# Performance work log

Hardware: AMD Instinct MI355X
Metric: run time of the kernel (lower is better)

Reference implementation:

```python
import jax, jax.numpy as jnp
import numpy as np

ODE_UNFOLDS = 6
EPS = 1e-8


def setup_inputs() -> dict:
    key = jax.random.key(0)
    ks = jax.random.split(key, 16)
    B, T, IN, U = 256, 128, 64, 256

    def unif(k, shape, lo, hi):
        return jax.random.uniform(k, shape, jnp.float32, lo, hi)

    def pm1(k, shape):  # random +/-1 reversal potentials (as in ncps erev init)
        return (2.0 * jax.random.bernoulli(k, 0.5, shape) - 1.0).astype(jnp.float32)

    return {
        "x_ltc": jax.random.normal(ks[0], (B, T, IN), jnp.float32),
        "timespans": jnp.ones((B, T, 1), jnp.float32),
        # sensory synapses (input -> units)
        "sensory_mu": unif(ks[1], (IN, U), 0.3, 0.8),
        "sensory_sigma": unif(ks[2], (IN, U), 3.0, 8.0),
        "sensory_w": unif(ks[3], (IN, U), 0.001, 1.0),
        "sensory_erev": pm1(ks[4], (IN, U)),
        # recurrent synapses (units -> units)
        "mu": unif(ks[5], (U, U), 0.3, 0.8),
        "sigma": unif(ks[6], (U, U), 3.0, 8.0),
        "w": unif(ks[7], (U, U), 0.001, 1.0),
        "erev": pm1(ks[8], (U, U)),
        # per-neuron leak / capacitance
        "gleak": unif(ks[9], (U,), 0.001, 1.0),
        "vleak": unif(ks[10], (U,), -0.2, 0.2),
        "cm": unif(ks[11], (U,), 0.4, 0.6),
        # affine input / output mappings
        "input_w": jnp.ones((IN,), jnp.float32),
        "input_b": jnp.zeros((IN,), jnp.float32),
        "output_w": jnp.ones((U,), jnp.float32),
        "output_b": jnp.zeros((U,), jnp.float32),
        # head: Linear(hidden, 1)
        "head_w": jax.random.normal(ks[12], (1, U), jnp.float32) * 0.05,
        "head_b": jnp.zeros((1,), jnp.float32),
    }


def reference(x_ltc, timespans, sensory_mu, sensory_sigma, sensory_w, sensory_erev,
              mu, sigma, w, erev, gleak, vleak, cm,
              input_w, input_b, output_w, output_b, head_w, head_b):
    B = x_ltc.shape[0]
    U = gleak.shape[0]

    def gate(v, mu_, sigma_):
        # v: (B, pre) -> (B, pre, post) sigmoid activation
        return jax.nn.sigmoid(sigma_ * (v[:, :, None] - mu_))

    def cell(v, xt, elapsed):
        x = xt * input_w + input_b                              # (B, IN)
        s_act = sensory_w * gate(x, sensory_mu, sensory_sigma)  # (B, IN, U)
        w_num_s = jnp.sum(s_act * sensory_erev, axis=1)          # (B, U)
        w_den_s = jnp.sum(s_act, axis=1)                         # (B, U)
        cm_t = cm / (elapsed / ODE_UNFOLDS)                      # (B, U) via (B,1) bcast
        for _ in range(ODE_UNFOLDS):                             # semi-implicit Euler unfolds
            w_act = w * gate(v, mu, sigma)                       # (B, U, U)
            w_num = jnp.sum(w_act * erev, axis=1) + w_num_s
            w_den = jnp.sum(w_act, axis=1) + w_den_s
            num = cm_t * v + gleak * vleak + w_num
            den = cm_t + gleak + w_den
            v = num / (den + EPS)
        return v

    def step(v, inp):
        xt, el = inp
        return cell(v, xt, el), None

    v0 = jnp.zeros((B, U), x_ltc.dtype)
    xs = (jnp.swapaxes(x_ltc, 0, 1), jnp.swapaxes(timespans, 0, 1))  # (T,B,IN), (T,B,1)
    vT, _ = jax.lax.scan(step, v0, xs)
    h_out = vT * output_w + output_b                             # output mapping of last step
    return h_out @ head_w.T + head_b                             # (B, 1)
```

## Files before the change

kernel.cpp:

```cpp
#include <hip/hip_runtime.h>
#include <hip/hip_bf16.h>
#include <hip/hip_fp16.h>

#define LOG2E 1.4426950408889634f

constexpr int B_ = 256, T_ = 128, IN_ = 64, U_ = 256;
constexpr int UNFOLDS = 6;

constexpr size_t OFF_RCD = 0;
constexpr size_t OFF_RWS = 262144;
constexpr size_t OFF_SCD = 393216;
constexpr size_t OFF_SWS = 458752;
constexpr size_t OFF_ELF = 491520;
constexpr size_t OFF_VEC = 622592;

typedef _Float16 hv2 __attribute__((ext_vector_type(2)));

__device__ __forceinline__ float ldf(const void* p, int idx, bool isbf) {
  return isbf ? __bfloat162float(((const __hip_bfloat16*)p)[idx])
              : ((const float*)p)[idx];
}

__device__ __forceinline__ float fdot2f(__half2 a, __half2 b, float c) {
#if __has_builtin(__builtin_amdgcn_fdot2)
  return __builtin_amdgcn_fdot2(__builtin_bit_cast(hv2, a),
                                __builtin_bit_cast(hv2, b), c, false);
#else
  return c + __low2float(a) * __low2float(b) +
         __high2float(a) * __high2float(b);
#endif
}

__device__ __forceinline__ unsigned packpair(float lo, float hi) {
  return __builtin_bit_cast(unsigned, __builtin_amdgcn_cvt_pkrtz(lo, hi));
}

__global__ __launch_bounds__(256) void ltc_prep(
    const void* tspan, const void* smu, const void* ssigma, const void* sw,
    const void* serev, const void* mu, const void* sigma, const void* w,
    const void* erev, const void* gleak, const void* vleak, const void* cm,
    const void* inw, const void* inb, const void* outw, const void* outb,
    const void* headw, const void* headb, char* __restrict__ ws) {
  const bool isbf = (((const unsigned*)tspan)[0] == 0x3F803F80u);
  const int idx = blockIdx.x * blockDim.x + threadIdx.x;

  uint2*    rcd = (uint2*)(ws + OFF_RCD);
  unsigned* rws = (unsigned*)(ws + OFF_RWS);
  uint2*    scd = (uint2*)(ws + OFF_SCD);
  unsigned* sws = (unsigned*)(ws + OFF_SWS);
  float*    elf = (float*)(ws + OFF_ELF);
  float*    vec = (float*)(ws + OFF_VEC);

  if (idx < (U_ * U_) / 2) {
    const int j = idx & 255, P = idx >> 8;
    const int e0 = (2 * P) * U_ + j, e1 = (2 * P + 1) * U_ + j;
    float sg0 = ldf(sigma, e0, isbf), m0 = ldf(mu, e0, isbf);
    float w0  = ldf(w, e0, isbf),     er0 = ldf(erev, e0, isbf);
    float sg1 = ldf(sigma, e1, isbf), m1 = ldf(mu, e1, isbf);
    float w1  = ldf(w, e1, isbf),     er1 = ldf(erev, e1, isbf);
    __half2 C, D, W;
    C.x = __float2half_rn(sg0 * m0 * LOG2E);  C.y = __float2half_rn(sg1 * m1 * LOG2E);
    D.x = __float2half_rn(-sg0 * LOG2E);      D.y = __float2half_rn(-sg1 * LOG2E);
    W.x = __float2half_rn(w0 * er0);          W.y = __float2half_rn(w1 * er1);
    rcd[P * 256 + j] = make_uint2(__builtin_bit_cast(unsigned, C),
                                  __builtin_bit_cast(unsigned, D));
    rws[P * 256 + j] = __builtin_bit_cast(unsigned, W);
  }
  if (idx < (IN_ * U_) / 2) {
    const int j = idx & 255, P = idx >> 8;
    const int e0 = (2 * P) * U_ + j, e1 = (2 * P + 1) * U_ + j;
    float sg0 = ldf(ssigma, e0, isbf), m0 = ldf(smu, e0, isbf);
    float w0  = ldf(sw, e0, isbf),     er0 = ldf(serev, e0, isbf);
    float sg1 = ldf(ssigma, e1, isbf), m1 = ldf(smu, e1, isbf);
    float w1  = ldf(sw, e1, isbf),     er1 = ldf(serev, e1, isbf);
    __half2 C, D, W;
    C.x = __float2half_rn(sg0 * m0 * LOG2E);  C.y = __float2half_rn(sg1 * m1 * LOG2E);
    D.x = __float2half_rn(-sg0 * LOG2E);      D.y = __float2half_rn(-sg1 * LOG2E);
    W.x = __float2half_rn(w0 * er0);          W.y = __float2half_rn(w1 * er1);
    scd[P * 256 + j] = make_uint2(__builtin_bit_cast(unsigned, C),
                                  __builtin_bit_cast(unsigned, D));
    sws[P * 256 + j] = __builtin_bit_cast(unsigned, W);
  }
  if (idx < B_ * T_) elf[idx] = ldf(tspan, idx, isbf);
  if (idx < U_) {
    float gl = ldf(gleak, idx, isbf);
    float hw = ldf(headw, idx, isbf);
    vec[idx]        = gl;
    vec[256 + idx]  = gl * ldf(vleak, idx, isbf);
    vec[512 + idx]  = ldf(cm, idx, isbf);
    vec[768 + idx]  = ldf(outw, idx, isbf) * hw;
    vec[1024 + idx] = ldf(outb, idx, isbf) * hw;
  }
  if (idx < IN_) {
    vec[1280 + idx] = ldf(inw, idx, isbf);
    vec[1344 + idx] = ldf(inb, idx, isbf);
  }
  if (idx == 0) vec[1408] = ldf(headb, 0, isbf);
}

__device__ __forceinline__ void pairj(unsigned uC, unsigned uD, unsigned uW,
                                      unsigned uV, __half2 one2,
                                      float& n, float& d) {
  const __half2 C  = __builtin_bit_cast(__half2, uC);
  const __half2 D  = __builtin_bit_cast(__half2, uD);
  const __half2 W  = __builtin_bit_cast(__half2, uW);
  const __half2 Wa = __builtin_bit_cast(__half2, uW & 0x7fff7fffu);
  const __half2 vh = __builtin_bit_cast(__half2, uV);
  __half2 th = __hfma2(D, vh, C);
  __half2 eh = h2exp2(th);
  __half2 ph = __hadd2(eh, one2);
  __half2 rh = h2rcp(ph);
  n = fdot2f(W, rh, n);
  d = fdot2f(Wa, rh, d);
}

__global__ __launch_bounds__(1024, 4) void ltc_main(
    const void* __restrict__ x_ltc, const void* __restrict__ tspan,
    const char* __restrict__ ws, void* __restrict__ out) {
  __shared__ uint2    s_cd[8192];
  __shared__ unsigned s_ws[8192];
  __shared__ float2 redA[4][257];
  __shared__ float2 redS[4][257];
  __shared__ __attribute__((aligned(16))) unsigned vh_sh[2][U_ / 2];
  __shared__ unsigned xh_sh[2][IN_ / 2];
  __shared__ float el_sh[T_];
  __shared__ float red[1024];

  const bool isbf = (((const unsigned*)tspan)[0] == 0x3F803F80u);
  const int b   = blockIdx.x;
  const int tid = threadIdx.x;
  const int j   = tid & 255;
  const int gq  = tid >> 8;

  const uint2*    rcd2 = (const uint2*)(ws + OFF_RCD);
  const unsigned* rws1 = (const unsigned*)(ws + OFF_RWS);
  const uint2*    scd2 = (const uint2*)(ws + OFF_SCD);
  const unsigned* sws1 = (const unsigned*)(ws + OFF_SWS);
  const float*    elf  = (const float*)(ws + OFF_ELF);
  const float*    vec  = (const float*)(ws + OFF_VEC);

  for (int i = tid; i < 8192; i += 1024) { s_cd[i] = scd2[i]; s_ws[i] = sws1[i]; }

  const float r_gl   = vec[j];
  const float r_glvl = vec[256 + j];
  const float r_cm6  = vec[512 + j] * (float)UNFOLDS;
  float vj = 0.f;

  if (tid < T_) el_sh[tid] = elf[b * T_ + tid];
  if (tid < U_ / 2) vh_sh[0][tid] = 0u;

  const int xl = tid - 768;
  float r_iw0 = 0.f, r_iw1 = 0.f, r_ib0 = 0.f, r_ib1 = 0.f;
  if (xl >= 0 && xl < IN_ / 2) {
    r_iw0 = vec[1280 + 2 * xl]; r_iw1 = vec[1280 + 2 * xl + 1];
    r_ib0 = vec[1344 + 2 * xl]; r_ib1 = vec[1344 + 2 * xl + 1];
    float x0 = ldf(x_ltc, (b * T_ + 0) * IN_ + 2 * xl, isbf);
    float x1 = ldf(x_ltc, (b * T_ + 0) * IN_ + 2 * xl + 1, isbf);
    xh_sh[0][xl] = packpair(fmaf(x0, r_iw0, r_ib0), fmaf(x1, r_iw1, r_ib1));
  }
  __syncthreads();

  __half2 one2;
  one2.x = __float2half_rn(1.0f);
  one2.y = one2.x;

  float SN = 0.f, SD = 0.f, cmt = 0.f;
  int cur = 0;

#pragma unroll 1
  for (int t = 0; t < T_; ++t) {
    {
      const unsigned* xc = xh_sh[t & 1];
      float sn = 0.f, sd = 0.f;
#pragma unroll
      for (int m = 0; m < 8; ++m) {
        const int P = gq * 8 + m;
        uint2 cd = s_cd[P * 256 + j];
        pairj(cd.x, cd.y, s_ws[P * 256 + j], xc[P], one2, sn, sd);
      }
      redS[gq][j] = make_float2(sn, sd);
    }

#pragma unroll 1
    for (int u = 0; u < UNFOLDS; ++u) {
      {
        const uint4* vh4 = (const uint4*)vh_sh[cur];
        float n = 0.f, d = 0.f;
        const int e0 = (gq * 32) * 256 + j;
        uint2 pc0 = rcd2[e0],       pc1 = rcd2[e0 + 256];
        uint2 pc2 = rcd2[e0 + 512], pc3 = rcd2[e0 + 768];
        unsigned pw0 = rws1[e0],       pw1 = rws1[e0 + 256];
        unsigned pw2 = rws1[e0 + 512], pw3 = rws1[e0 + 768];
#pragma unroll
        for (int mm = 0; mm < 8; ++mm) {
          uint2 c0 = pc0, c1 = pc1, c2 = pc2, c3 = pc3;
          unsigned w0 = pw0, w1 = pw1, w2 = pw2, w3 = pw3;
          if (mm < 7) {
            const int e = (gq * 32 + (mm + 1) * 4) * 256 + j;
            pc0 = rcd2[e];       pc1 = rcd2[e + 256];
            pc2 = rcd2[e + 512]; pc3 = rcd2[e + 768];
            pw0 = rws1[e];       pw1 = rws1[e + 256];
            pw2 = rws1[e + 512]; pw3 = rws1[e + 768];
          }
          uint4 vv = vh4[gq * 8 + mm];
          pairj(c0.x, c0.y, w0, vv.x, one2, n, d);
          pairj(c1.x, c1.y, w1, vv.y, one2, n, d);
          pairj(c2.x, c2.y, w2, vv.z, one2, n, d);
          pairj(c3.x, c3.y, w3, vv.w, one2, n, d);
        }
        redA[gq][j] = make_float2(n, d);
      }
      if (u == UNFOLDS - 1 && xl >= 0 && xl < IN_ / 2 && t + 1 < T_) {
        float x0 = ldf(x_ltc, (b * T_ + t + 1) * IN_ + 2 * xl, isbf);
        float x1 = ldf(x_ltc, (b * T_ + t + 1) * IN_ + 2 * xl + 1, isbf);
        xh_sh[(t + 1) & 1][xl] =
            packpair(fmaf(x0, r_iw0, r_ib0), fmaf(x1, r_iw1, r_ib1));
      }
      __syncthreads();

      if (u == 0) {
        float2 s0 = redS[0][j], s1 = redS[1][j], s2 = redS[2][j], s3 = redS[3][j];
        SN = s0.x + s1.x + s2.x + s3.x;
        SD = s0.y + s1.y + s2.y + s3.y;
        cmt = r_cm6 * __builtin_amdgcn_rcpf(el_sh[t]);
      }
      {
        float2 a0 = redA[0][j], a1 = redA[1][j], a2 = redA[2][j], a3 = redA[3][j];
        float n = a0.x + a1.x + a2.x + a3.x + SN;
        float d = a0.y + a1.y + a2.y + a3.y + SD;
        float vnew = (fmaf(cmt, vj, r_glvl) + n) *
                     __builtin_amdgcn_rcpf(cmt + r_gl + d + 1e-8f);
        vj = vnew;
        float vo = __shfl_xor(vnew, 1);
        if (tid < U_ && (tid & 1) == 0)
          vh_sh[cur ^ 1][tid >> 1] = packpair(vnew, vo);
      }
      __syncthreads();
      cur ^= 1;
    }
  }

  float val = 0.f;
  if (tid < U_) val = fmaf(vj, vec[768 + tid], vec[1024 + tid]);
  red[tid] = val;
  __syncthreads();
  for (int s = 512; s > 0; s >>= 1) {
    if (tid < s) red[tid] += red[tid + s];
    __syncthreads();
  }
  if (tid == 0) {
    float o = red[0] + vec[1408];
    if (isbf) ((__hip_bfloat16*)out)[b] = __float2bfloat16(o);
    else      ((float*)out)[b] = o;
  }
}

extern "C" void kernel_launch(void* const* d_in, const int* in_sizes, int n_in,
                              void* d_out, int out_size, void* d_ws, size_t ws_size,
                              hipStream_t stream) {
  (void)in_sizes; (void)n_in; (void)out_size; (void)ws_size;
  const void* x_ltc  = d_in[0];
  const void* tspan  = d_in[1];
  const void* smu    = d_in[2];
  const void* ssigma = d_in[3];
  const void* sw     = d_in[4];
  const void* serev  = d_in[5];
  const void* mu     = d_in[6];
  const void* sigma  = d_in[7];
  const void* w      = d_in[8];
  const void* erev   = d_in[9];
  const void* gleak  = d_in[10];
  const void* vleak  = d_in[11];
  const void* cmv    = d_in[12];
  const void* inw    = d_in[13];
  const void* inb    = d_in[14];
  const void* outw   = d_in[15];
  const void* outb   = d_in[16];
  const void* headw  = d_in[17];
  const void* headb  = d_in[18];

  ltc_prep<<<128, 256, 0, stream>>>(
      tspan, smu, ssigma, sw, serev, mu, sigma, w, erev,
      gleak, vleak, cmv, inw, inb, outw, outb, headw, headb, (char*)d_ws);

  ltc_main<<<B_, 1024, 0, stream>>>(x_ltc, tspan, (const char*)d_ws, d_out);
}
```

Measured before the change: 3.919 ms.

## Remap threads so 4 lanes share a neuron, cache recurrent params in LDS

Threads are remapped so the four partial sums for each post-neuron sit in adjacent lanes and are reduced with shuffles. This removes the shared-memory reduction arrays and one __syncthreads per unfold. Sensory parameters move into registers, which frees LDS to hold 12 of the 32 recurrent parameter chunks instead of re-reading them from global memory every unfold. The workspace layout is permuted to match. In exchange, LDS use and register pressure go up, which could limit occupancy.

```diff
diff --git a/kernel.cpp b/kernel.cpp
--- a/kernel.cpp
+++ b/kernel.cpp
@@ -6,6 +6,7 @@
 
 constexpr int B_ = 256, T_ = 128, IN_ = 64, U_ = 256;
 constexpr int UNFOLDS = 6;
+constexpr int NST = 12;
 
 constexpr size_t OFF_RCD = 0;
 constexpr size_t OFF_RWS = 262144;
@@ -62,9 +63,11 @@
     C.x = __float2half_rn(sg0 * m0 * LOG2E);  C.y = __float2half_rn(sg1 * m1 * LOG2E);
     D.x = __float2half_rn(-sg0 * LOG2E);      D.y = __float2half_rn(-sg1 * LOG2E);
     W.x = __float2half_rn(w0 * er0);          W.y = __float2half_rn(w1 * er1);
-    rcd[P * 256 + j] = make_uint2(__builtin_bit_cast(unsigned, C),
-                                  __builtin_bit_cast(unsigned, D));
-    rws[P * 256 + j] = __builtin_bit_cast(unsigned, W);
+    const int gq = P >> 5, m = P & 31;
+    const int dst = m * 1024 + j * 4 + gq;
+    rcd[dst] = make_uint2(__builtin_bit_cast(unsigned, C),
+                          __builtin_bit_cast(unsigned, D));
+    rws[dst] = __builtin_bit_cast(unsigned, W);
   }
   if (idx < (IN_ * U_) / 2) {
     const int j = idx & 255, P = idx >> 8;
@@ -77,9 +80,11 @@
     C.x = __float2half_rn(sg0 * m0 * LOG2E);  C.y = __float2half_rn(sg1 * m1 * LOG2E);
     D.x = __float2half_rn(-sg0 * LOG2E);      D.y = __float2half_rn(-sg1 * LOG2E);
     W.x = __float2half_rn(w0 * er0);          W.y = __float2half_rn(w1 * er1);
-    scd[P * 256 + j] = make_uint2(__builtin_bit_cast(unsigned, C),
-                                  __builtin_bit_cast(unsigned, D));
-    sws[P * 256 + j] = __builtin_bit_cast(unsigned, W);
+    const int gq = P >> 3, m = P & 7;
+    const int dst = m * 1024 + j * 4 + gq;
+    scd[dst] = make_uint2(__builtin_bit_cast(unsigned, C),
+                          __builtin_bit_cast(unsigned, D));
+    sws[dst] = __builtin_bit_cast(unsigned, W);
   }
   if (idx < B_ * T_) elf[idx] = ldf(tspan, idx, isbf);
   if (idx < U_) {
@@ -114,13 +119,16 @@
   d = fdot2f(Wa, rh, d);
 }
 
+__device__ __forceinline__ void bfly4(float& n, float& d) {
+  n += __shfl_xor(n, 1); d += __shfl_xor(d, 1);
+  n += __shfl_xor(n, 2); d += __shfl_xor(d, 2);
+}
+
 __global__ __launch_bounds__(1024, 4) void ltc_main(
     const void* __restrict__ x_ltc, const void* __restrict__ tspan,
     const char* __restrict__ ws, void* __restrict__ out) {
-  __shared__ uint2    s_cd[8192];
-  __shared__ unsigned s_ws[8192];
-  __shared__ float2 redA[4][257];
-  __shared__ float2 redS[4][257];
+  __shared__ uint2    l_cd[NST * 1024];
+  __shared__ unsigned l_ws[NST * 1024];
   __shared__ __attribute__((aligned(16))) unsigned vh_sh[2][U_ / 2];
   __shared__ unsigned xh_sh[2][IN_ / 2];
   __shared__ float el_sh[T_];
@@ -129,8 +137,9 @@
   const bool isbf = (((const unsigned*)tspan)[0] == 0x3F803F80u);
   const int b   = blockIdx.x;
   const int tid = threadIdx.x;
-  const int j   = tid & 255;
-  const int gq  = tid >> 8;
+  const int j   = tid >> 2;
+  const int gq  = tid & 3;
+  (void)gq;
 
   const uint2*    rcd2 = (const uint2*)(ws + OFF_RCD);
   const unsigned* rws1 = (const unsigned*)(ws + OFF_RWS);
@@ -139,7 +148,18 @@
   const float*    elf  = (const float*)(ws + OFF_ELF);
   const float*    vec  = (const float*)(ws + OFF_VEC);
 
-  for (int i = tid; i < 8192; i += 1024) { s_cd[i] = scd2[i]; s_ws[i] = sws1[i]; }
+  for (int i = tid; i < NST * 1024; i += 1024) {
+    l_cd[i] = rcd2[i];
+    l_ws[i] = rws1[i];
+  }
+
+  uint2    sc[8];
+  unsigned swr[8];
+#pragma unroll
+  for (int m = 0; m < 8; ++m) {
+    sc[m]  = scd2[m * 1024 + tid];
+    swr[m] = sws1[m * 1024 + tid];
+  }
 
   const float r_gl   = vec[j];
   const float r_glvl = vec[256 + j];
@@ -164,84 +184,81 @@
   one2.x = __float2half_rn(1.0f);
   one2.y = one2.x;
 
-  float SN = 0.f, SD = 0.f, cmt = 0.f;
   int cur = 0;
 
 #pragma unroll 1
   for (int t = 0; t < T_; ++t) {
+    float SN, SD;
     {
       const unsigned* xc = xh_sh[t & 1];
       float sn = 0.f, sd = 0.f;
 #pragma unroll
-      for (int m = 0; m < 8; ++m) {
-        const int P = gq * 8 + m;
-        uint2 cd = s_cd[P * 256 + j];
-        pairj(cd.x, cd.y, s_ws[P * 256 + j], xc[P], one2, sn, sd);
-      }
-      redS[gq][j] = make_float2(sn, sd);
+      for (int m = 0; m < 8; ++m)
+        pairj(sc[m].x, sc[m].y, swr[m], xc[gq * 8 + m], one2, sn, sd);
+      bfly4(sn, sd);
+      SN = sn; SD = sd;
     }
+    const float cmt = r_cm6 * __builtin_amdgcn_rcpf(el_sh[t]);
 
 #pragma unroll 1
     for (int u = 0; u < UNFOLDS; ++u) {
-      {
-        const uint4* vh4 = (const uint4*)vh_sh[cur];
-        float n = 0.f, d = 0.f;
-        const int e0 = (gq * 32) * 256 + j;
-        uint2 pc0 = rcd2[e0],       pc1 = rcd2[e0 + 256];
-        uint2 pc2 = rcd2[e0 + 512], pc3 = rcd2[e0 + 768];
-        unsigned pw0 = rws1[e0],       pw1 = rws1[e0 + 256];
-        unsigned pw2 = rws1[e0 + 512], pw3 = rws1[e0 + 768];
+      const uint4* vh4 = (const uint4*)vh_sh[cur];
+      float n = 0.f, d = 0.f;
+
+      const int eg0 = 12 * 1024 + tid;
+      uint2 pc0 = rcd2[eg0],            pc1 = rcd2[eg0 + 1024];
+      uint2 pc2 = rcd2[eg0 + 2048],     pc3 = rcd2[eg0 + 3072];
+      unsigned pw0 = rws1[eg0],         pw1 = rws1[eg0 + 1024];
+      unsigned pw2 = rws1[eg0 + 2048],  pw3 = rws1[eg0 + 3072];
+
 #pragma unroll
-        for (int mm = 0; mm < 8; ++mm) {
-          uint2 c0 = pc0, c1 = pc1, c2 = pc2, c3 = pc3;
-          unsigned w0 = pw0, w1 = pw1, w2 = pw2, w3 = pw3;
-          if (mm < 7) {
-            const int e = (gq * 32 + (mm + 1) * 4) * 256 + j;
-            pc0 = rcd2[e];       pc1 = rcd2[e + 256];
-            pc2 = rcd2[e + 512]; pc3 = rcd2[e + 768];
-            pw0 = rws1[e];       pw1 = rws1[e + 256];
-            pw2 = rws1[e + 512]; pw3 = rws1[e + 768];
-          }
-          uint4 vv = vh4[gq * 8 + mm];
-          pairj(c0.x, c0.y, w0, vv.x, one2, n, d);
-          pairj(c1.x, c1.y, w1, vv.y, one2, n, d);
-          pairj(c2.x, c2.y, w2, vv.z, one2, n, d);
-          pairj(c3.x, c3.y, w3, vv.w, one2, n, d);
+      for (int mm = 0; mm < 3; ++mm) {
+        uint4 vv = vh4[gq * 8 + mm];
+        const int e = (4 * mm) * 1024 + tid;
+        pairj(l_cd[e].x,        l_cd[e].y,        l_ws[e],        vv.x, one2, n, d);
+        pairj(l_cd[e + 1024].x, l_cd[e + 1024].y, l_ws[e + 1024], vv.y, one2, n, d);
+        pairj(l_cd[e + 2048].x, l_cd[e + 2048].y, l_ws[e + 2048], vv.z, one2, n, d);
+        pairj(l_cd[e + 3072].x, l_cd[e + 3072].y, l_ws[e + 3072], vv.w, one2, n, d);
+      }
+#pragma unroll
+      for (int mm = 3; mm < 8; ++mm) {
+        uint2 c0 = pc0, c1 = pc1, c2 = pc2, c3 = pc3;
+        unsigned w0 = pw0, w1 = pw1, w2 = pw2, w3 = pw3;
+        if (mm < 7) {
+          const int e = (4 * (mm + 1)) * 1024 + tid;
+          pc0 = rcd2[e];        pc1 = rcd2[e + 1024];
+          pc2 = rcd2[e + 2048]; pc3 = rcd2[e + 3072];
+          pw0 = rws1[e];        pw1 = rws1[e + 1024];
+          pw2 = rws1[e + 2048]; pw3 = rws1[e + 3072];
         }
-        redA[gq][j] = make_float2(n, d);
+        uint4 vv = vh4[gq * 8 + mm];
+        pairj(c0.x, c0.y, w0, vv.x, one2, n, d);
+        pairj(c1.x, c1.y, w1, vv.y, one2, n, d);
+        pairj(c2.x, c2.y, w2, vv.z, one2, n, d);
+        pairj(c3.x, c3.y, w3, vv.w, one2, n, d);
       }
+
       if (u == UNFOLDS - 1 && xl >= 0 && xl < IN_ / 2 && t + 1 < T_) {
         float x0 = ldf(x_ltc, (b * T_ + t + 1) * IN_ + 2 * xl, isbf);
         float x1 = ldf(x_ltc, (b * T_ + t + 1) * IN_ + 2 * xl + 1, isbf);
         xh_sh[(t + 1) & 1][xl] =
             packpair(fmaf(x0, r_iw0, r_ib0), fmaf(x1, r_iw1, r_ib1));
       }
-      __syncthreads();
-
-      if (u == 0) {
-        float2 s0 = redS[0][j], s1 = redS[1][j], s2 = redS[2][j], s3 = redS[3][j];
-        SN = s0.x + s1.x + s2.x + s3.x;
-        SD = s0.y + s1.y + s2.y + s3.y;
-        cmt = r_cm6 * __builtin_amdgcn_rcpf(el_sh[t]);
-      }
-      {
-        float2 a0 = redA[0][j], a1 = redA[1][j], a2 = redA[2][j], a3 = redA[3][j];
-        float n = a0.x + a1.x + a2.x + a3.x + SN;
-        float d = a0.y + a1.y + a2.y + a3.y + SD;
-        float vnew = (fmaf(cmt, vj, r_glvl) + n) *
-                     __builtin_amdgcn_rcpf(cmt + r_gl + d + 1e-8f);
-        vj = vnew;
-        float vo = __shfl_xor(vnew, 1);
-        if (tid < U_ && (tid & 1) == 0)
-          vh_sh[cur ^ 1][tid >> 1] = packpair(vnew, vo);
-      }
+
+      bfly4(n, d);
+      n += SN; d += SD;
+      float vnew = (fmaf(cmt, vj, r_glvl) + n) *
+                   __builtin_amdgcn_rcpf(cmt + r_gl + d + 1e-8f);
+      vj = vnew;
+      float vo = __shfl_xor(vnew, 4);
+      if ((tid & 7) == 0) vh_sh[cur ^ 1][tid >> 3] = packpair(vnew, vo);
       __syncthreads();
       cur ^= 1;
     }
   }
 
   float val = 0.f;
-  if (tid < U_) val = fmaf(vj, vec[768 + tid], vec[1024 + tid]);
+  if ((tid & 3) == 0) val = fmaf(vj, vec[768 + j], vec[1024 + j]);
   red[tid] = val;
   __syncthreads();
   for (int s = 512; s > 0; s >>= 1) {
```

After: 5.245 ms. 33.8% more time.
